# Performance work log

Measured on AMD Instinct MI355X. Metric: run time of the kernel, lower is better.

## Reference

```python
import jax, jax.numpy as jnp
import numpy as np

WINDOW_SIZE = 11
SIGMA = 1.5

def _gaussian_window():
    x = np.arange(WINDOW_SIZE, dtype=np.float64) - WINDOW_SIZE // 2
    g = np.exp(-(x ** 2) / (2.0 * SIGMA ** 2))
    g = (g / g.sum()).astype(np.float32)
    w2 = np.outer(g, g)  # [11, 11]
    return jnp.asarray(w2)


def setup_inputs() -> dict:
    key = jax.random.key(0)
    k1, k2 = jax.random.split(key)
    B, C, H, W = 32, 3, 512, 512
    img1 = jax.random.uniform(k1, (B, C, H, W), dtype=jnp.float32)
    img2 = jax.random.uniform(k2, (B, C, H, W), dtype=jnp.float32)
    return {"img1": img1, "img2": img2}


def reference(img1, img2):
    # peak = 1.0, size_average = True
    c1 = jnp.float32(0.01 ** 2)
    c2 = jnp.float32(0.03 ** 2)
    C = img1.shape[1]
    w2 = _gaussian_window()

    # One fused depthwise conv over the 5 statistic planes (same math as 5
    # separate grouped convs in the original).
    stacked = jnp.concatenate(
        [img1, img2, img1 * img1, img2 * img2, img1 * img2], axis=1
    )  # [B, 5C, H, W]
    kernel = jnp.tile(w2[None, None], (5 * C, 1, 1, 1))  # [5C, 1, 11, 11]
    out = jax.lax.conv_general_dilated(
        stacked, kernel,
        window_strides=(1, 1), padding='VALID',
        feature_group_count=5 * C,
        dimension_numbers=('NCHW', 'OIHW', 'NCHW'),
    )  # [B, 5C, H-10, W-10]

    mu1 = out[:, 0 * C:1 * C]
    mu2 = out[:, 1 * C:2 * C]
    mu1_sq = mu1 * mu1
    mu2_sq = mu2 * mu2
    mu1_mu2 = mu1 * mu2
    sigma1_sq = out[:, 2 * C:3 * C] - mu1_sq
    sigma2_sq = out[:, 3 * C:4 * C] - mu2_sq
    sigma12 = out[:, 4 * C:5 * C] - mu1_mu2

    ssim_map = ((2 * mu1_mu2 + c1) * (2 * sigma12 + c2)) / (
        (mu1_sq + mu2_sq + c1) * (sigma1_sq + sigma2_sq + c2)
    )
    return jnp.mean(ssim_map)
```

## Files before the change

### kernel.cpp

```cpp
#include <hip/hip_runtime.h>


namespace {
constexpr int IMG_H = 512;
constexpr int IMG_W = 512;
constexpr int NIMG  = 96;
constexpr int OUT_H = 502;
constexpr int OUT_W = 502;
constexpr int RPB   = 32;
constexpr int QR    = 2;
constexpr int BUFW  = 544;
constexpr double TOTAL = 24192384.0;

constexpr double U0 = 0.0038659201;
constexpr double U1 = 0.0285655007;
constexpr double U2 = 0.1353352832366127;
constexpr double U3 = 0.4111122898;
constexpr double U4 = 0.8007374026;
constexpr double S  = 1.0 + 2.0 * (U0 + U1 + U2 + U3 + U4);
}

__device__ __forceinline__ float2 f2fma(float w, float2 a, float2 c) {
    return make_float2(fmaf(w, a.x, c.x), fmaf(w, a.y, c.y));
}

__global__ __launch_bounds__(256, 3) void ssim_main(const float* __restrict__ img1,
                                                    const float* __restrict__ img2,
                                                    double* __restrict__ acc)
{
    __shared__ __align__(16) float vrow[QR][5][BUFW];
    __shared__ float red[4];

    const float g[11] = {
        (float)(U0/S), (float)(U1/S), (float)(U2/S), (float)(U3/S), (float)(U4/S),
        (float)(1.0/S),
        (float)(U4/S), (float)(U3/S), (float)(U2/S), (float)(U1/S), (float)(U0/S)
    };
    constexpr float C1 = 1e-4f;
    constexpr float C2 = 9e-4f;

    const int t   = threadIdx.x;
    const int z   = blockIdx.y;
    const int oy0 = blockIdx.x * RPB;
    const int row_end = min(oy0 + RPB, OUT_H);

    const float2* p1 = (const float2*)(img1 + (size_t)z * (IMG_H * IMG_W)) + t;
    const float2* p2 = (const float2*)(img2 + (size_t)z * (IMG_H * IMG_W)) + t;

    const int c4w  = t >> 1;
    const int woff = ((c4w ^ ((c4w >> 3) & 7)) << 2) + ((t & 1) << 1);

    const int hq = t >> 7;
    const int cb = (t & 127) << 2;
    int roff[4];
    #pragma unroll
    for (int k = 0; k < 4; ++k) {
        int c4 = (cb >> 2) + k;
        roff[k] = (c4 ^ ((c4 >> 3) & 7)) << 2;
    }

    float local = 0.f;

    for (int r0 = oy0; r0 < row_end; r0 += QR) {
        float2 vm1[QR], vm2[QR], v11[QR], v22[QR], v12[QR];
        #pragma unroll
        for (int q = 0; q < QR; ++q) {
            vm1[q] = make_float2(0.f, 0.f);
            vm2[q] = make_float2(0.f, 0.f);
            v11[q] = make_float2(0.f, 0.f);
            v22[q] = make_float2(0.f, 0.f);
            v12[q] = make_float2(0.f, 0.f);
        }
        #pragma unroll
        for (int j = 0; j < QR + 10; ++j) {
            const float2 x = p1[(r0 + j) * (IMG_W / 2)];
            const float2 y = p2[(r0 + j) * (IMG_W / 2)];
            const float2 xx = make_float2(x.x * x.x, x.y * x.y);
            const float2 yy = make_float2(y.x * y.x, y.y * y.y);
            const float2 xy = make_float2(x.x * y.x, x.y * y.y);
            #pragma unroll
            for (int q = 0; q < QR; ++q) {
                const int k = j - q;
                if (k >= 0 && k < 11) {
                    const float w = g[k];
                    vm1[q] = f2fma(w, x,  vm1[q]);
                    vm2[q] = f2fma(w, y,  vm2[q]);
                    v11[q] = f2fma(w, xx, v11[q]);
                    v22[q] = f2fma(w, yy, v22[q]);
                    v12[q] = f2fma(w, xy, v12[q]);
                }
            }
        }
        __syncthreads();
        #pragma unroll
        for (int q = 0; q < QR; ++q) {
            *(float2*)&vrow[q][0][woff] = vm1[q];
            *(float2*)&vrow[q][1][woff] = vm2[q];
            *(float2*)&vrow[q][2][woff] = v11[q];
            *(float2*)&vrow[q][3][woff] = v22[q];
            *(float2*)&vrow[q][4][woff] = v12[q];
        }
        __syncthreads();

        const int rr = r0 + hq;
        if (rr < row_end) {
            float aa[5][4];
            #pragma unroll
            for (int ch = 0; ch < 5; ++ch) {
                const float* bc = &vrow[hq][ch][0];
                float f[16];
                #pragma unroll
                for (int k = 0; k < 4; ++k) {
                    float4 v = *(const float4*)(bc + roff[k]);
                    f[4*k+0] = v.x; f[4*k+1] = v.y; f[4*k+2] = v.z; f[4*k+3] = v.w;
                }
                #pragma unroll
                for (int j = 0; j < 4; ++j) {
                    float s = 0.f;
                    #pragma unroll
                    for (int k = 0; k < 11; ++k) s = fmaf(g[k], f[j + k], s);
                    aa[ch][j] = s;
                }
            }
            #pragma unroll
            for (int j = 0; j < 4; ++j) {
                if (cb + j < OUT_W) {
                    float mu1 = aa[0][j], mu2 = aa[1][j];
                    float e11 = aa[2][j], e22 = aa[3][j], e12 = aa[4][j];
                    float mu11 = mu1 * mu1;
                    float mu22 = mu2 * mu2;
                    float mu12 = mu1 * mu2;
                    float s1  = e11 - mu11;
                    float s2  = e22 - mu22;
                    float s12 = e12 - mu12;
                    float num = fmaf(2.f, mu12, C1) * fmaf(2.f, s12, C2);
                    float den = (mu11 + mu22 + C1) * (s1 + s2 + C2);
                    local = fmaf(num, __builtin_amdgcn_rcpf(den), local);
                }
            }
        }
    }

    #pragma unroll
    for (int off = 32; off > 0; off >>= 1) local += __shfl_down(local, off, 64);
    if ((t & 63) == 0) red[t >> 6] = local;
    __syncthreads();
    if (t == 0) {
        double s = (double)red[0] + (double)red[1] + (double)red[2] + (double)red[3];
        atomicAdd(acc, s);
    }
}

__global__ void ssim_fin(const double* __restrict__ acc, float* __restrict__ out)
{
    out[0] = (float)(acc[0] / TOTAL);
}

extern "C" void kernel_launch(void* const* d_in, const int* in_sizes, int n_in,
                              void* d_out, int out_size, void* d_ws, size_t ws_size,
                              hipStream_t stream)
{
    (void)in_sizes; (void)n_in; (void)out_size; (void)ws_size;
    const float* img1 = (const float*)d_in[0];
    const float* img2 = (const float*)d_in[1];
    double* acc = (double*)d_ws;

    hipMemsetAsync(d_ws, 0, sizeof(double), stream);
    dim3 grid((OUT_H + RPB - 1) / RPB, NIMG);
    hipLaunchKernelGGL(ssim_main, grid, dim3(256), 0, stream, img1, img2, acc);
    hipLaunchKernelGGL(ssim_fin, dim3(1), dim3(1), 0, stream, acc, (float*)d_out);
}
```

Measured before the change: 293.3 us.

## Merge squared-stat planes, double-buffer shared rows, and enlarge row blocks

Convolves x²+y² as a single plane instead of separate x² and y² planes, since only their sum enters the denominator. This cuts the blurred channels from five to four, reducing FMAs and shared-memory traffic. The shared row buffer is double-buffered by parity, which removes one barrier per iteration. Rows per block are doubled, lowering grid size and per-block overhead at the cost of fewer blocks for load balance.

```diff
diff --git a/kernel.cpp b/kernel.cpp
--- a/kernel.cpp
+++ b/kernel.cpp
@@ -7,7 +7,7 @@
 constexpr int NIMG  = 96;
 constexpr int OUT_H = 502;
 constexpr int OUT_W = 502;
-constexpr int RPB   = 32;
+constexpr int RPB   = 64;
 constexpr int QR    = 2;
 constexpr int BUFW  = 544;
 constexpr double TOTAL = 24192384.0;
@@ -28,7 +28,7 @@
                                                     const float* __restrict__ img2,
                                                     double* __restrict__ acc)
 {
-    __shared__ __align__(16) float vrow[QR][5][BUFW];
+    __shared__ __align__(16) float vrow[2][QR][4][BUFW];
     __shared__ float red[4];
 
     const float g[11] = {
@@ -60,54 +60,51 @@
     }
 
     float local = 0.f;
+    int p = 0;
 
-    for (int r0 = oy0; r0 < row_end; r0 += QR) {
-        float2 vm1[QR], vm2[QR], v11[QR], v22[QR], v12[QR];
+    for (int r0 = oy0; r0 < row_end; r0 += QR, p ^= 1) {
+        float2 am1[QR], am2[QR], app[QR], axy[QR];
         #pragma unroll
         for (int q = 0; q < QR; ++q) {
-            vm1[q] = make_float2(0.f, 0.f);
-            vm2[q] = make_float2(0.f, 0.f);
-            v11[q] = make_float2(0.f, 0.f);
-            v22[q] = make_float2(0.f, 0.f);
-            v12[q] = make_float2(0.f, 0.f);
+            am1[q] = make_float2(0.f, 0.f);
+            am2[q] = make_float2(0.f, 0.f);
+            app[q] = make_float2(0.f, 0.f);
+            axy[q] = make_float2(0.f, 0.f);
         }
         #pragma unroll
         for (int j = 0; j < QR + 10; ++j) {
             const float2 x = p1[(r0 + j) * (IMG_W / 2)];
             const float2 y = p2[(r0 + j) * (IMG_W / 2)];
-            const float2 xx = make_float2(x.x * x.x, x.y * x.y);
-            const float2 yy = make_float2(y.x * y.x, y.y * y.y);
+            const float2 pp = make_float2(fmaf(x.x, x.x, y.x * y.x),
+                                          fmaf(x.y, x.y, y.y * y.y));
             const float2 xy = make_float2(x.x * y.x, x.y * y.y);
             #pragma unroll
             for (int q = 0; q < QR; ++q) {
                 const int k = j - q;
                 if (k >= 0 && k < 11) {
                     const float w = g[k];
-                    vm1[q] = f2fma(w, x,  vm1[q]);
-                    vm2[q] = f2fma(w, y,  vm2[q]);
-                    v11[q] = f2fma(w, xx, v11[q]);
-                    v22[q] = f2fma(w, yy, v22[q]);
-                    v12[q] = f2fma(w, xy, v12[q]);
+                    am1[q] = f2fma(w, x,  am1[q]);
+                    am2[q] = f2fma(w, y,  am2[q]);
+                    app[q] = f2fma(w, pp, app[q]);
+                    axy[q] = f2fma(w, xy, axy[q]);
                 }
             }
         }
-        __syncthreads();
         #pragma unroll
         for (int q = 0; q < QR; ++q) {
-            *(float2*)&vrow[q][0][woff] = vm1[q];
-            *(float2*)&vrow[q][1][woff] = vm2[q];
-            *(float2*)&vrow[q][2][woff] = v11[q];
-            *(float2*)&vrow[q][3][woff] = v22[q];
-            *(float2*)&vrow[q][4][woff] = v12[q];
+            *(float2*)&vrow[p][q][0][woff] = am1[q];
+            *(float2*)&vrow[p][q][1][woff] = am2[q];
+            *(float2*)&vrow[p][q][2][woff] = app[q];
+            *(float2*)&vrow[p][q][3][woff] = axy[q];
         }
         __syncthreads();
 
         const int rr = r0 + hq;
         if (rr < row_end) {
-            float aa[5][4];
+            float aa[4][4];
             #pragma unroll
-            for (int ch = 0; ch < 5; ++ch) {
-                const float* bc = &vrow[hq][ch][0];
+            for (int ch = 0; ch < 4; ++ch) {
+                const float* bc = &vrow[p][hq][ch][0];
                 float f[16];
                 #pragma unroll
                 for (int k = 0; k < 4; ++k) {
@@ -126,15 +123,15 @@
             for (int j = 0; j < 4; ++j) {
                 if (cb + j < OUT_W) {
                     float mu1 = aa[0][j], mu2 = aa[1][j];
-                    float e11 = aa[2][j], e22 = aa[3][j], e12 = aa[4][j];
+                    float ee  = aa[2][j], e12 = aa[3][j];
                     float mu11 = mu1 * mu1;
                     float mu22 = mu2 * mu2;
                     float mu12 = mu1 * mu2;
-                    float s1  = e11 - mu11;
-                    float s2  = e22 - mu22;
-                    float s12 = e12 - mu12;
+                    float mm   = mu11 + mu22;
+                    float s12  = e12 - mu12;
+                    float spp  = ee - mm;
                     float num = fmaf(2.f, mu12, C1) * fmaf(2.f, s12, C2);
-                    float den = (mu11 + mu22 + C1) * (s1 + s2 + C2);
+                    float den = (mm + C1) * (spp + C2);
                     local = fmaf(num, __builtin_amdgcn_rcpf(den), local);
                 }
             }
```

Result: no change. 288.6 us (-1.6%).
